# Performance work log

Hardware: AMD Instinct MI355X
Metric: run time of the kernel (lower is better)

## Reference

```python
import jax, jax.numpy as jnp
import numpy as np

D_MODEL = 1024
NUM_HEADS = 16
HEAD_DIM = D_MODEL // NUM_HEADS


def setup_inputs() -> dict:
    key = jax.random.key(0)
    ks = jax.random.split(key, 9)
    s = 1.0 / np.sqrt(D_MODEL)
    x = jax.random.normal(ks[0], (2, 2048, D_MODEL), dtype=jnp.float32)
    Wq = jax.random.normal(ks[1], (D_MODEL, D_MODEL), dtype=jnp.float32) * s
    bq = jnp.zeros((D_MODEL,), dtype=jnp.float32)
    Wk = jax.random.normal(ks[2], (D_MODEL, D_MODEL), dtype=jnp.float32) * s
    bk = jnp.zeros((D_MODEL,), dtype=jnp.float32)
    Wv = jax.random.normal(ks[3], (D_MODEL, D_MODEL), dtype=jnp.float32) * s
    bv = jnp.zeros((D_MODEL,), dtype=jnp.float32)
    Wo = jax.random.normal(ks[4], (D_MODEL, D_MODEL), dtype=jnp.float32) * s
    bo = jnp.zeros((D_MODEL,), dtype=jnp.float32)
    return {"x": x, "Wq": Wq, "bq": bq, "Wk": Wk, "bk": bk,
            "Wv": Wv, "bv": bv, "Wo": Wo, "bo": bo}


def reference(x, Wq, bq, Wk, bk, Wv, bv, Wo, bo):
    B, S, D = x.shape
    H, Hd = NUM_HEADS, HEAD_DIM
    scale = 1.0 / np.sqrt(Hd)

    def split_heads(t):  # [B,S,D] -> [B,H,S,Hd]
        return t.reshape(B, S, H, Hd).transpose(0, 2, 1, 3)

    q = split_heads(x @ Wq + bq)
    k = split_heads(x @ Wk + bk)
    v = split_heads(x @ Wv + bv)

    scores = jnp.einsum('bhqd,bhkd->bhqk', q, k) * scale
    scores = scores - jnp.max(scores, axis=-1, keepdims=True)
    attn = jax.nn.softmax(scores, axis=-1)
    attended = jnp.einsum('bhqk,bhkd->bhqd', attn, v)
    attended = attended.transpose(0, 2, 1, 3).reshape(B, S, D)
    return attended @ Wo + bo
```

## Files before the change

### kernel.cpp

```cpp
#include <hip/hip_runtime.h>
#include <hip/hip_bf16.h>

typedef __bf16 bf16_t;
typedef __bf16 bf16x8 __attribute__((ext_vector_type(8)));
typedef __bf16 bf16x4 __attribute__((ext_vector_type(4)));
typedef float floatx4 __attribute__((ext_vector_type(4)));
typedef short short4v __attribute__((ext_vector_type(4)));

#define D_MODEL 1024
#define SEQ     2048
#define BATCH   2
#define NHEAD   16
#define HDIM    64
#define MTOT    (BATCH * SEQ)

#define QSCALE  0.18033688011112042f

union PBu { bf16x4 b; short4v s; };

__device__ __forceinline__ void async_copy16(const bf16_t* g, bf16_t* l) {
    __builtin_amdgcn_global_load_lds(
        (const __attribute__((address_space(1))) void*)g,
        (__attribute__((address_space(3))) void*)l, 16, 0, 0);
}

__global__ void cvt_f32_bf16(const float* __restrict__ x, bf16_t* __restrict__ y, int n) {
    int i = (blockIdx.x * 256 + threadIdx.x) * 4;
    if (i < n) {
        const float4 v = *(const float4*)(x + i);
        bf16x4 o = { (bf16_t)v.x, (bf16_t)v.y, (bf16_t)v.z, (bf16_t)v.w };
        *(bf16x4*)(y + i) = o;
    }
}

__global__ void transpose_w4(
    const float* __restrict__ W0, const float* __restrict__ W1,
    const float* __restrict__ W2, const float* __restrict__ W3,
    bf16_t* __restrict__ T0, bf16_t* __restrict__ T1,
    bf16_t* __restrict__ T2, bf16_t* __restrict__ T3)
{
    __shared__ float tile[32][33];
    const int z = blockIdx.z;
    const float* W = (z == 0) ? W0 : (z == 1) ? W1 : (z == 2) ? W2 : W3;
    bf16_t*     Wt = (z == 0) ? T0 : (z == 1) ? T1 : (z == 2) ? T2 : T3;
    const int tx = threadIdx.x, ty = threadIdx.y;
    const int k0 = blockIdx.y * 32, n0 = blockIdx.x * 32;
#pragma unroll
    for (int j = 0; j < 32; j += 8)
        tile[ty + j][tx] = W[(size_t)(k0 + ty + j) * D_MODEL + n0 + tx];
    __syncthreads();
#pragma unroll
    for (int j = 0; j < 32; j += 8)
        Wt[(size_t)(n0 + ty + j) * D_MODEL + k0 + tx] = (bf16_t)tile[tx][ty + j];
}

__device__ __forceinline__ void gemm_mainloop(
    const bf16_t* __restrict__ A, const bf16_t* __restrict__ Bt,
    int m0, int n0, bf16_t* As, bf16_t* Bs, floatx4 acc[4][4])
{
    const int tid  = threadIdx.x;
    const int lane = tid & 63;
    const int wid  = tid >> 6;
    const int quad = lane >> 4;
    const int col  = lane & 15;
    const int wm   = (wid >> 1) * 64;
    const int wn   = (wid & 1) * 64;
    const int srow = tid >> 3;
    const int scc  = ((tid & 7) ^ (srow & 7)) * 8;
    const int xorc = col & 7;

    const bf16_t* Ag = A  + (size_t)(m0 + srow) * D_MODEL + scc;
    const bf16_t* Bg = Bt + (size_t)(n0 + srow) * D_MODEL + scc;
    bf16_t* Al = As + tid * 8;
    bf16_t* Bl = Bs + tid * 8;

    for (int kb = 0; kb < D_MODEL; kb += 64) {
#pragma unroll
        for (int p = 0; p < 4; ++p) {
            async_copy16(Ag + kb + p * (32 * D_MODEL), Al + p * 2048);
            async_copy16(Bg + kb + p * (32 * D_MODEL), Bl + p * 2048);
        }
        __syncthreads();
#pragma unroll
        for (int kh = 0; kh < 2; ++kh) {
            bf16x8 af[4], bfr[4];
#pragma unroll
            for (int i = 0; i < 4; ++i)
                af[i] = *(const bf16x8*)(As + (wm + i * 16 + col) * 64 + (((kh * 4 + quad) ^ xorc) * 8));
#pragma unroll
            for (int j = 0; j < 4; ++j)
                bfr[j] = *(const bf16x8*)(Bs + (wn + j * 16 + col) * 64 + (((kh * 4 + quad) ^ xorc) * 8));
#pragma unroll
            for (int i = 0; i < 4; ++i)
#pragma unroll
                for (int j = 0; j < 4; ++j)
                    acc[i][j] = __builtin_amdgcn_mfma_f32_16x16x32_bf16(af[i], bfr[j], acc[i][j], 0, 0, 0);
        }
        __syncthreads();
    }
}

__global__ __launch_bounds__(256, 3) void gemm_qkv(
    const bf16_t* __restrict__ xb,
    const bf16_t* __restrict__ Wtq, const bf16_t* __restrict__ Wtk, const bf16_t* __restrict__ Wtv,
    const float* __restrict__ bq, const float* __restrict__ bk, const float* __restrict__ bv,
    bf16_t* __restrict__ Q, bf16_t* __restrict__ Kh, bf16_t* __restrict__ Vt)
{
    __shared__ bf16_t As[128 * 64];
    __shared__ bf16_t Bs[128 * 64];
    const int z = blockIdx.z;
    const bf16_t* Bt   = (z == 0) ? Wtq : (z == 1) ? Wtk : Wtv;
    const float*  bias = (z == 0) ? bq  : (z == 1) ? bk  : bv;
    bf16_t*       O    = (z == 0) ? Q   : (z == 1) ? Kh  : Vt;
    const float   qs   = (z == 0) ? QSCALE : 1.0f;
    const int m0 = blockIdx.y * 128;
    const int n0 = blockIdx.x * 128;

    floatx4 acc[4][4];
#pragma unroll
    for (int i = 0; i < 4; ++i)
#pragma unroll
        for (int j = 0; j < 4; ++j)
            acc[i][j] = (floatx4){0.f, 0.f, 0.f, 0.f};

    gemm_mainloop(xb, Bt, m0, n0, As, Bs, acc);

    const int tid  = threadIdx.x;
    const int lane = tid & 63;
    const int wid  = tid >> 6;
    const int quad = lane >> 4;
    const int col  = lane & 15;
    const int wm   = (wid >> 1) * 64;
    const int wn   = (wid & 1) * 64;

    if (z == 2) {
#pragma unroll
        for (int i = 0; i < 4; ++i) {
#pragma unroll
            for (int j = 0; j < 4; ++j) {
                const int n = n0 + wn + j * 16 + col;
                const float bb = bias[n];
                const int mb = m0 + wm + i * 16 + quad * 4;
                const size_t bhb = (size_t)((mb >> 11) * NHEAD + (n >> 6)) * (SEQ * HDIM);
                bf16x4 pk = { (bf16_t)(acc[i][j][0] + bb), (bf16_t)(acc[i][j][1] + bb),
                              (bf16_t)(acc[i][j][2] + bb), (bf16_t)(acc[i][j][3] + bb) };
                *(bf16x4*)(O + bhb + (size_t)(n & 63) * SEQ + (mb & 2047)) = pk;
            }
        }
    } else {
#pragma unroll
        for (int i = 0; i < 4; ++i) {
#pragma unroll
            for (int j = 0; j < 4; ++j) {
                const int n = n0 + wn + j * 16 + col;
                const float bb = bias[n];
#pragma unroll
                for (int r = 0; r < 4; ++r) {
                    const int m = m0 + wm + i * 16 + quad * 4 + r;
                    const float v = (acc[i][j][r] + bb) * qs;
                    const size_t bhb = (size_t)((m >> 11) * NHEAD + (n >> 6)) * (SEQ * HDIM);
                    O[bhb + (size_t)(m & 2047) * HDIM + (n & 63)] = (bf16_t)v;
                }
            }
        }
    }
}

__global__ __launch_bounds__(256, 4) void attn_kernel(
    const bf16_t* __restrict__ Q, const bf16_t* __restrict__ K,
    const bf16_t* __restrict__ Vt, bf16_t* __restrict__ A2)
{
    __shared__ bf16_t Ks[64 * 64];
    __shared__ bf16_t Vs[64 * 64];

    const int tid  = threadIdx.x;
    const int lane = tid & 63;
    const int wid  = tid >> 6;
    const int quad = lane >> 4;
    const int col  = lane & 15;
    const int xorc = col & 7;

    const int blk = blockIdx.x;
    const int idx = blk >> 3;
    const int bh  = (blk & 7) * 4 + (idx >> 5);
    const int q0  = (idx & 31) * 64;
    const int b   = bh >> 4, h = bh & 15;

    const bf16_t* Qb = Q  + (size_t)bh * (SEQ * HDIM);
    const bf16_t* Kb = K  + (size_t)bh * (SEQ * HDIM);
    const bf16_t* Vb = Vt + (size_t)bh * (SEQ * HDIM);

    const int qrow = q0 + wid * 16 + col;
    bf16x8 qf0 = *(const bf16x8*)(Qb + (size_t)qrow * HDIM + quad * 8);
    bf16x8 qf1 = *(const bf16x8*)(Qb + (size_t)qrow * HDIM + 32 + quad * 8);

    floatx4 o_acc[4];
    float lsum = 0.f;
#pragma unroll
    for (int dt = 0; dt < 4; ++dt)
        o_acc[dt] = (floatx4){0.f, 0.f, 0.f, 0.f};

    const int srow = tid >> 3;
    const int scc  = ((tid & 7) ^ (srow & 7)) * 8;
    const bf16_t* Kg = Kb + (size_t)srow * HDIM + scc;
    const bf16_t* Vg = Vb + (size_t)srow * SEQ + scc;
    bf16_t* KsL = Ks + tid * 8;
    bf16_t* VsL = Vs + tid * 8;

    for (int it = 0; it < 32; ++it) {
        const int ko = it * 64;
        async_copy16(Kg + (size_t)ko * HDIM, KsL);
        async_copy16(Kg + (size_t)(ko + 32) * HDIM, KsL + 2048);
        async_copy16(Vg + ko, VsL);
        async_copy16(Vg + (size_t)32 * SEQ + ko, VsL + 2048);
        __syncthreads();

        bf16x8 kf[4][2];
#pragma unroll
        for (int t = 0; t < 4; ++t) {
            kf[t][0] = *(const bf16x8*)(Ks + (t * 16 + col) * 64 + ((quad ^ xorc) * 8));
            kf[t][1] = *(const bf16x8*)(Ks + (t * 16 + col) * 64 + (((4 + quad) ^ xorc) * 8));
        }
        short4v vfr[4][4];
#pragma unroll
        for (int dt = 0; dt < 4; ++dt)
#pragma unroll
            for (int t = 0; t < 4; ++t) {
                const int sch = t * 2 + (quad >> 1);
                vfr[dt][t] = *(const short4v*)(Vs + (dt * 16 + col) * 64 + ((sch ^ xorc) * 8) + (quad & 1) * 4);
            }

        floatx4 s_acc[4];
        short4v pb[4];
#pragma unroll
        for (int t = 0; t < 4; ++t) {
            s_acc[t] = (floatx4){0.f, 0.f, 0.f, 0.f};
            s_acc[t] = __builtin_amdgcn_mfma_f32_16x16x32_bf16(kf[t][0], qf0, s_acc[t], 0, 0, 0);
            s_acc[t] = __builtin_amdgcn_mfma_f32_16x16x32_bf16(kf[t][1], qf1, s_acc[t], 0, 0, 0);
        }
#pragma unroll
        for (int t = 0; t < 4; ++t) {
            const float p0 = __builtin_amdgcn_exp2f(s_acc[t][0]);
            const float p1 = __builtin_amdgcn_exp2f(s_acc[t][1]);
            const float p2 = __builtin_amdgcn_exp2f(s_acc[t][2]);
            const float p3 = __builtin_amdgcn_exp2f(s_acc[t][3]);
            lsum += (p0 + p1) + (p2 + p3);
            PBu u;
            u.b = (bf16x4){ (bf16_t)p0, (bf16_t)p1, (bf16_t)p2, (bf16_t)p3 };
            pb[t] = u.s;
        }
#pragma unroll
        for (int dt = 0; dt < 4; ++dt)
#pragma unroll
            for (int t = 0; t < 4; ++t)
                o_acc[dt] = __builtin_amdgcn_mfma_f32_16x16x16bf16_1k(vfr[dt][t], pb[t], o_acc[dt], 0, 0, 0);
        __syncthreads();
    }

    lsum += __shfl_xor(lsum, 16, 64);
    lsum += __shfl_xor(lsum, 32, 64);
    const float inv = 1.0f / lsum;

    bf16_t* dst = A2 + ((size_t)(b * SEQ + qrow)) * D_MODEL + h * HDIM + quad * 4;
#pragma unroll
    for (int dt = 0; dt < 4; ++dt) {
        bf16x4 pk = { (bf16_t)(o_acc[dt][0] * inv), (bf16_t)(o_acc[dt][1] * inv),
                      (bf16_t)(o_acc[dt][2] * inv), (bf16_t)(o_acc[dt][3] * inv) };
        *(bf16x4*)(dst + dt * 16) = pk;
    }
}

__global__ __launch_bounds__(256, 3) void gemm_proj(
    const bf16_t* __restrict__ A2, const bf16_t* __restrict__ Wto,
    const float* __restrict__ bo, float* __restrict__ out)
{
    __shared__ bf16_t As[64 * 64];
    __shared__ bf16_t Bs[128 * 64];
    const int m0 = blockIdx.y * 64;
    const int n0 = blockIdx.x * 128;

    const int tid  = threadIdx.x;
    const int lane = tid & 63;
    const int wid  = tid >> 6;
    const int quad = lane >> 4;
    const int col  = lane & 15;
    const int wm   = (wid >> 1) * 32;
    const int wn   = (wid & 1) * 64;
    const int srow = tid >> 3;
    const int scc  = ((tid & 7) ^ (srow & 7)) * 8;
    const int xorc = col & 7;

    floatx4 acc[2][4];
#pragma unroll
    for (int i = 0; i < 2; ++i)
#pragma unroll
        for (int j = 0; j < 4; ++j)
            acc[i][j] = (floatx4){0.f, 0.f, 0.f, 0.f};

    const bf16_t* Ag = A2  + (size_t)(m0 + srow) * D_MODEL + scc;
    const bf16_t* Bg = Wto + (size_t)(n0 + srow) * D_MODEL + scc;
    bf16_t* Al = As + tid * 8;
    bf16_t* Bl = Bs + tid * 8;

    for (int kb = 0; kb < D_MODEL; kb += 64) {
#pragma unroll
        for (int p = 0; p < 2; ++p)
            async_copy16(Ag + kb + p * (32 * D_MODEL), Al + p * 2048);
#pragma unroll
        for (int p = 0; p < 4; ++p)
            async_copy16(Bg + kb + p * (32 * D_MODEL), Bl + p * 2048);
        __syncthreads();
#pragma unroll
        for (int kh = 0; kh < 2; ++kh) {
            bf16x8 af[2], bfr[4];
#pragma unroll
            for (int i = 0; i < 2; ++i)
                af[i] = *(const bf16x8*)(As + (wm + i * 16 + col) * 64 + (((kh * 4 + quad) ^ xorc) * 8));
#pragma unroll
            for (int j = 0; j < 4; ++j)
                bfr[j] = *(const bf16x8*)(Bs + (wn + j * 16 + col) * 64 + (((kh * 4 + quad) ^ xorc) * 8));
#pragma unroll
            for (int i = 0; i < 2; ++i)
#pragma unroll
                for (int j = 0; j < 4; ++j)
                    acc[i][j] = __builtin_amdgcn_mfma_f32_16x16x32_bf16(af[i], bfr[j], acc[i][j], 0, 0, 0);
        }
        __syncthreads();
    }

#pragma unroll
    for (int i = 0; i < 2; ++i) {
#pragma unroll
        for (int j = 0; j < 4; ++j) {
            const int n = n0 + wn + j * 16 + col;
            const float bb = bo[n];
#pragma unroll
            for (int r = 0; r < 4; ++r) {
                const int m = m0 + wm + i * 16 + quad * 4 + r;
                out[(size_t)m * D_MODEL + n] = acc[i][j][r] + bb;
            }
        }
    }
}

extern "C" void kernel_launch(void* const* d_in, const int* in_sizes, int n_in,
                              void* d_out, int out_size, void* d_ws, size_t ws_size,
                              hipStream_t stream) {
    const float* x  = (const float*)d_in[0];
    const float* Wq = (const float*)d_in[1];
    const float* bq = (const float*)d_in[2];
    const float* Wk = (const float*)d_in[3];
    const float* bk = (const float*)d_in[4];
    const float* Wv = (const float*)d_in[5];
    const float* bv = (const float*)d_in[6];
    const float* Wo = (const float*)d_in[7];
    const float* bo = (const float*)d_in[8];
    float* out = (float*)d_out;

    const size_t MB = 1ull << 20;
    char* ws = (char*)d_ws;
    bf16_t* Q     = (bf16_t*)(ws + 0 * MB);
    bf16_t* Kh    = (bf16_t*)(ws + 8 * MB);
    bf16_t* Vt    = (bf16_t*)(ws + 16 * MB);
    bf16_t* A2    = (bf16_t*)(ws + 24 * MB);
    bf16_t* xb    = (bf16_t*)(ws + 32 * MB);
    bf16_t* Wtq   = (bf16_t*)(ws + 40 * MB);
    bf16_t* Wtk   = (bf16_t*)(ws + 42 * MB);
    bf16_t* Wtv   = (bf16_t*)(ws + 44 * MB);
    bf16_t* Wto   = (bf16_t*)(ws + 46 * MB);

    const int nx = MTOT * D_MODEL;
    cvt_f32_bf16<<<nx / (256 * 4), 256, 0, stream>>>(x, xb, nx);

    transpose_w4<<<dim3(D_MODEL / 32, D_MODEL / 32, 4), dim3(32, 8), 0, stream>>>(
        Wq, Wk, Wv, Wo, Wtq, Wtk, Wtv, Wto);

    gemm_qkv<<<dim3(D_MODEL / 128, MTOT / 128, 3), 256, 0, stream>>>(
        xb, Wtq, Wtk, Wtv, bq, bk, bv, Q, Kh, Vt);

    attn_kernel<<<dim3(1024), 256, 0, stream>>>(Q, Kh, Vt, A2);

    gemm_proj<<<dim3(D_MODEL / 128, MTOT / 64), 256, 0, stream>>>(A2, Wto, bo, out);
}
```

Measured before the change: 191.7 us.

## Double-buffer K/V tiles and process 128 query rows per attention block

```diff
diff --git a/kernel.cpp b/kernel.cpp
--- a/kernel.cpp
+++ b/kernel.cpp
@@ -166,12 +166,12 @@
     }
 }
 
-__global__ __launch_bounds__(256, 4) void attn_kernel(
+__global__ __launch_bounds__(256, 2) void attn_kernel(
     const bf16_t* __restrict__ Q, const bf16_t* __restrict__ K,
     const bf16_t* __restrict__ Vt, bf16_t* __restrict__ A2)
 {
-    __shared__ bf16_t Ks[64 * 64];
-    __shared__ bf16_t Vs[64 * 64];
+    __shared__ bf16_t Ks[2][64 * 64];
+    __shared__ bf16_t Vs[2][64 * 64];
 
     const int tid  = threadIdx.x;
     const int lane = tid & 63;
@@ -182,44 +182,52 @@
 
     const int blk = blockIdx.x;
     const int idx = blk >> 3;
-    const int bh  = (blk & 7) * 4 + (idx >> 5);
-    const int q0  = (idx & 31) * 64;
+    const int bh  = (blk & 7) * 4 + (idx >> 4);
+    const int q0  = (idx & 15) * 128;
     const int b   = bh >> 4, h = bh & 15;
 
     const bf16_t* Qb = Q  + (size_t)bh * (SEQ * HDIM);
     const bf16_t* Kb = K  + (size_t)bh * (SEQ * HDIM);
     const bf16_t* Vb = Vt + (size_t)bh * (SEQ * HDIM);
 
-    const int qrow = q0 + wid * 16 + col;
-    bf16x8 qf0 = *(const bf16x8*)(Qb + (size_t)qrow * HDIM + quad * 8);
-    bf16x8 qf1 = *(const bf16x8*)(Qb + (size_t)qrow * HDIM + 32 + quad * 8);
-
-    floatx4 o_acc[4];
-    float lsum = 0.f;
-#pragma unroll
-    for (int dt = 0; dt < 4; ++dt)
-        o_acc[dt] = (floatx4){0.f, 0.f, 0.f, 0.f};
+    bf16x8 qf[2][2];
+#pragma unroll
+    for (int g = 0; g < 2; ++g) {
+        const int qrow = q0 + wid * 32 + g * 16 + col;
+        qf[g][0] = *(const bf16x8*)(Qb + (size_t)qrow * HDIM + quad * 8);
+        qf[g][1] = *(const bf16x8*)(Qb + (size_t)qrow * HDIM + 32 + quad * 8);
+    }
+
+    floatx4 o_acc[2][4];
+    float lsum[2] = {0.f, 0.f};
+#pragma unroll
+    for (int g = 0; g < 2; ++g)
+#pragma unroll
+        for (int dt = 0; dt < 4; ++dt)
+            o_acc[g][dt] = (floatx4){0.f, 0.f, 0.f, 0.f};
 
     const int srow = tid >> 3;
     const int scc  = ((tid & 7) ^ (srow & 7)) * 8;
     const bf16_t* Kg = Kb + (size_t)srow * HDIM + scc;
     const bf16_t* Vg = Vb + (size_t)srow * SEQ + scc;
-    bf16_t* KsL = Ks + tid * 8;
-    bf16_t* VsL = Vs + tid * 8;
-
-    for (int it = 0; it < 32; ++it) {
-        const int ko = it * 64;
-        async_copy16(Kg + (size_t)ko * HDIM, KsL);
-        async_copy16(Kg + (size_t)(ko + 32) * HDIM, KsL + 2048);
-        async_copy16(Vg + ko, VsL);
-        async_copy16(Vg + (size_t)32 * SEQ + ko, VsL + 2048);
-        __syncthreads();
-
+    bf16_t* KsL0 = &Ks[0][0] + tid * 8;
+    bf16_t* KsL1 = &Ks[1][0] + tid * 8;
+    bf16_t* VsL0 = &Vs[0][0] + tid * 8;
+    bf16_t* VsL1 = &Vs[1][0] + tid * 8;
+
+    auto stage = [&](int ko, bf16_t* dk, bf16_t* dv) {
+        async_copy16(Kg + (size_t)ko * HDIM, dk);
+        async_copy16(Kg + (size_t)(ko + 32) * HDIM, dk + 2048);
+        async_copy16(Vg + ko, dv);
+        async_copy16(Vg + (size_t)32 * SEQ + ko, dv + 2048);
+    };
+
+    auto step = [&](const bf16_t* KsC, const bf16_t* VsC) {
         bf16x8 kf[4][2];
 #pragma unroll
         for (int t = 0; t < 4; ++t) {
-            kf[t][0] = *(const bf16x8*)(Ks + (t * 16 + col) * 64 + ((quad ^ xorc) * 8));
-            kf[t][1] = *(const bf16x8*)(Ks + (t * 16 + col) * 64 + (((4 + quad) ^ xorc) * 8));
+            kf[t][0] = *(const bf16x8*)(KsC + (t * 16 + col) * 64 + ((quad ^ xorc) * 8));
+            kf[t][1] = *(const bf16x8*)(KsC + (t * 16 + col) * 64 + (((4 + quad) ^ xorc) * 8));
         }
         short4v vfr[4][4];
 #pragma unroll
@@ -227,46 +235,79 @@
 #pragma unroll
             for (int t = 0; t < 4; ++t) {
                 const int sch = t * 2 + (quad >> 1);
-                vfr[dt][t] = *(const short4v*)(Vs + (dt * 16 + col) * 64 + ((sch ^ xorc) * 8) + (quad & 1) * 4);
-            }
-
-        floatx4 s_acc[4];
-        short4v pb[4];
-#pragma unroll
-        for (int t = 0; t < 4; ++t) {
-            s_acc[t] = (floatx4){0.f, 0.f, 0.f, 0.f};
-            s_acc[t] = __builtin_amdgcn_mfma_f32_16x16x32_bf16(kf[t][0], qf0, s_acc[t], 0, 0, 0);
-            s_acc[t] = __builtin_amdgcn_mfma_f32_16x16x32_bf16(kf[t][1], qf1, s_acc[t], 0, 0, 0);
-        }
-#pragma unroll
-        for (int t = 0; t < 4; ++t) {
-            const float p0 = __builtin_amdgcn_exp2f(s_acc[t][0]);
-            const float p1 = __builtin_amdgcn_exp2f(s_acc[t][1]);
-            const float p2 = __builtin_amdgcn_exp2f(s_acc[t][2]);
-            const float p3 = __builtin_amdgcn_exp2f(s_acc[t][3]);
-            lsum += (p0 + p1) + (p2 + p3);
-            PBu u;
-            u.b = (bf16x4){ (bf16_t)p0, (bf16_t)p1, (bf16_t)p2, (bf16_t)p3 };
-            pb[t] = u.s;
-        }
-#pragma unroll
-        for (int dt = 0; dt < 4; ++dt)
-#pragma unroll
-            for (int t = 0; t < 4; ++t)
-                o_acc[dt] = __builtin_amdgcn_mfma_f32_16x16x16bf16_1k(vfr[dt][t], pb[t], o_acc[dt], 0, 0, 0);
-        __syncthreads();
-    }
-
-    lsum += __shfl_xor(lsum, 16, 64);
-    lsum += __shfl_xor(lsum, 32, 64);
-    const float inv = 1.0f / lsum;
-
-    bf16_t* dst = A2 + ((size_t)(b * SEQ + qrow)) * D_MODEL + h * HDIM + quad * 4;
-#pragma unroll
-    for (int dt = 0; dt < 4; ++dt) {
-        bf16x4 pk = { (bf16_t)(o_acc[dt][0] * inv), (bf16_t)(o_acc[dt][1] * inv),
-                      (bf16_t)(o_acc[dt][2] * inv), (bf16_t)(o_acc[dt][3] * inv) };
-        *(bf16x4*)(dst + dt * 16) = pk;
+                vfr[dt][t] = *(const short4v*)(VsC + (dt * 16 + col) * 64 + ((sch ^ xorc) * 8) + (quad & 1) * 4);
+            }
+#pragma unroll
+        for (int g = 0; g < 2; ++g) {
+            floatx4 s_acc[4];
+            short4v pb[4];
+#pragma unroll
+            for (int t = 0; t < 4; ++t) {
+                s_acc[t] = (floatx4){0.f, 0.f, 0.f, 0.f};
+                s_acc[t] = __builtin_amdgcn_mfma_f32_16x16x32_bf16(kf[t][0], qf[g][0], s_acc[t], 0, 0, 0);
+                s_acc[t] = __builtin_amdgcn_mfma_f32_16x16x32_bf16(kf[t][1], qf[g][1], s_acc[t], 0, 0, 0);
+            }
+            float ls = 0.f;
+#pragma unroll
+            for (int t = 0; t < 4; ++t) {
+                const float p0 = __builtin_amdgcn_exp2f(s_acc[t][0]);
+                const float p1 = __builtin_amdgcn_exp2f(s_acc[t][1]);
+                const float p2 = __builtin_amdgcn_exp2f(s_acc[t][2]);
+                const float p3 = __builtin_amdgcn_exp2f(s_acc[t][3]);
+                ls += (p0 + p1) + (p2 + p3);
+                PBu u;
+                u.b = (bf16x4){ (bf16_t)p0, (bf16_t)p1, (bf16_t)p2, (bf16_t)p3 };
+                pb[t] = u.s;
+            }
+            lsum[g] += ls;
+#pragma unroll
+            for (int dt = 0; dt < 4; ++dt)
+#pragma unroll
+                for (int t = 0; t < 4; ++t)
+                    o_acc[g][dt] = __builtin_amdgcn_mfma_f32_16x16x16bf16_1k(vfr[dt][t], pb[t], o_acc[g][dt], 0, 0, 0);
+        }
+    };
+
+    stage(0, KsL0, VsL0);
+    stage(64, KsL1, VsL1);
+
+#pragma unroll 1
+    for (int it2 = 0; it2 < 15; ++it2) {
+        asm volatile("s_waitcnt vmcnt(4)" ::: "memory");
+        __builtin_amdgcn_s_barrier();
+        step(&Ks[0][0], &Vs[0][0]);
+        asm volatile("s_waitcnt lgkmcnt(0)" ::: "memory");
+        __builtin_amdgcn_s_barrier();
+        stage((2 * it2 + 2) * 64, KsL0, VsL0);
+
+        asm volatile("s_waitcnt vmcnt(4)" ::: "memory");
+        __builtin_amdgcn_s_barrier();
+        step(&Ks[1][0], &Vs[1][0]);
+        asm volatile("s_waitcnt lgkmcnt(0)" ::: "memory");
+        __builtin_amdgcn_s_barrier();
+        stage((2 * it2 + 3) * 64, KsL1, VsL1);
+    }
+    asm volatile("s_waitcnt vmcnt(4)" ::: "memory");
+    __builtin_amdgcn_s_barrier();
+    step(&Ks[0][0], &Vs[0][0]);
+    asm volatile("s_waitcnt vmcnt(0)" ::: "memory");
+    __builtin_amdgcn_s_barrier();
+    step(&Ks[1][0], &Vs[1][0]);
+
+#pragma unroll
+    for (int g = 0; g < 2; ++g) {
+        float l = lsum[g];
+        l += __shfl_xor(l, 16, 64);
+        l += __shfl_xor(l, 32, 64);
+        const float inv = 1.0f / l;
+        const int qrow = q0 + wid * 32 + g * 16 + col;
+        bf16_t* dst = A2 + ((size_t)(b * SEQ + qrow)) * D_MODEL + h * HDIM + quad * 4;
+#pragma unroll
+        for (int dt = 0; dt < 4; ++dt) {
+            bf16x4 pk = { (bf16_t)(o_acc[g][dt][0] * inv), (bf16_t)(o_acc[g][dt][1] * inv),
+                          (bf16_t)(o_acc[g][dt][2] * inv), (bf16_t)(o_acc[g][dt][3] * inv) };
+            *(bf16x4*)(dst + dt * 16) = pk;
+        }
     }
 }
 
@@ -378,7 +419,7 @@
     gemm_qkv<<<dim3(D_MODEL / 128, MTOT / 128, 3), 256, 0, stream>>>(
         xb, Wtq, Wtk, Wtv, bq, bk, bv, Q, Kh, Vt);
 
-    attn_kernel<<<dim3(1024), 256, 0, stream>>>(Q, Kh, Vt, A2);
+    attn_kernel<<<dim3(512), 256, 0, stream>>>(Q, Kh, Vt, A2);
 
     gemm_proj<<<dim3(D_MODEL / 128, MTOT / 64), 256, 0, stream>>>(A2, Wto, bo, out);
 }
```

After: 187.6 us. -2.2%, faster.
